# Kernel optimization log

Hardware: AMD Instinct MI355X
Metric: run time of the kernel (lower is better)

Reference implementation:

```python
import jax, jax.numpy as jnp
import numpy as np

OUT, IN, BLK = 4096, 4096, 32
N_BLOCKS = OUT * IN // BLK
# FP4 magnitude lookup (E2M1): index = low 3 bits of the nibble
FP4_LOOKUP = jnp.array([0.0, 0.5, 1.0, 1.5, 2.0, 3.0, 4.0, 6.0], dtype=jnp.float32)


def setup_inputs() -> dict:
    key = jax.random.key(0)
    k1, k2, k3, k4 = jax.random.split(key, 4)
    x = jax.random.normal(k1, (4, 2048, IN), dtype=jnp.float32)
    # packed uint8 codes (stored as int32): two FP4 nibbles per byte
    quantized_weight = jax.random.randint(k2, (OUT * IN // 2,), 0, 256, dtype=jnp.int32)
    # positive per-block scales (abs-max of each 32-element block in the original)
    weight_scales = jax.random.uniform(k3, (N_BLOCKS,), dtype=jnp.float32, minval=0.01, maxval=1.0)
    bias = jax.random.normal(k4, (OUT,), dtype=jnp.float32) * 0.01
    return {"x": x, "quantized_weight": quantized_weight,
            "weight_scales": weight_scales, "bias": bias}


def _dequantize(quantized_weight, weight_scales):
    # unpack: high nibble first, then low nibble (matches _unpack_fp4 stack order)
    high = (quantized_weight >> 4) & 15
    low = quantized_weight & 15
    nibbles = jnp.stack([high, low], axis=-1).reshape(-1)  # [OUT*IN]
    # sign bit (bit 3): 1 -> negative, 0 -> positive
    sign = jnp.where(((nibbles >> 3) & 1) == 1, -1.0, 1.0).astype(jnp.float32)
    magnitude = FP4_LOOKUP[nibbles & 7]
    vals = magnitude * sign                                  # [OUT*IN]
    vals = vals.reshape(N_BLOCKS, BLK) * weight_scales[:, None]
    return vals.reshape(OUT, IN)


def reference(x, quantized_weight, weight_scales, bias):
    W = _dequantize(quantized_weight, weight_scales)  # [OUT, IN]
    # F.linear: x @ W.T + bias
    return jnp.einsum('bsi,oi->bso', x, W) + bias
```

## Files before the change

### kernel.cpp

```cpp
#include <hip/hip_runtime.h>
#include <hip/hip_bf16.h>
#include <stdint.h>


#define M_DIM 8192
#define N_DIM 4096
#define K_DIM 4096
#define NBLK_W (N_DIM * K_DIM / 32)

typedef __bf16 bf16x8 __attribute__((ext_vector_type(8)));
typedef float  f32x4  __attribute__((ext_vector_type(4)));


__device__ __forceinline__ uint16_t f32_to_bf16_rn(float f) {
  uint32_t u = __float_as_uint(f);
  uint32_t r = (u + 0x7FFFu + ((u >> 16) & 1u)) >> 16;
  return (uint16_t)r;
}
__device__ __forceinline__ uint32_t pack_bf16x2(float e0, float e1) {
  return (uint32_t)f32_to_bf16_rn(e0) | ((uint32_t)f32_to_bf16_rn(e1) << 16);
}
__device__ __forceinline__ float fp4_to_f32(int nib) {
  uint32_t e = (uint32_t)(nib >> 1) & 3u;
  uint32_t m = (uint32_t)nib & 1u;
  uint32_t s = (uint32_t)(nib >> 3) & 1u;
  uint32_t bits = e ? (((126u + e) << 23) | (m << 22)) : (m ? 0x3F000000u : 0u);
  bits |= s << 31;
  return __uint_as_float(bits);
}
__device__ __forceinline__ void gload_lds16(const void* g, void* lds) {
  __builtin_amdgcn_global_load_lds(
      (const __attribute__((address_space(1))) unsigned int*)g,
      (__attribute__((address_space(3))) unsigned int*)lds,
      16, 0, 0);
}

__global__ __launch_bounds__(256) void dequant_w(const int* __restrict__ q,
                                                 const float* __restrict__ scales,
                                                 uint32_t* __restrict__ W) {
  int b = blockIdx.x * 256 + threadIdx.x;
  float sc = scales[b];
  const int4* q4 = reinterpret_cast<const int4*>(q) + (size_t)b * 4;
  int4* dst = reinterpret_cast<int4*>(W + (size_t)b * 16);
#pragma unroll
  for (int i = 0; i < 4; ++i) {
    int4 v = q4[i];
    int b0 = v.x & 0xFF, b1 = v.y & 0xFF, b2 = v.z & 0xFF, b3 = v.w & 0xFF;
    uint32_t p0 = pack_bf16x2(fp4_to_f32((b0 >> 4) & 15) * sc, fp4_to_f32(b0 & 15) * sc);
    uint32_t p1 = pack_bf16x2(fp4_to_f32((b1 >> 4) & 15) * sc, fp4_to_f32(b1 & 15) * sc);
    uint32_t p2 = pack_bf16x2(fp4_to_f32((b2 >> 4) & 15) * sc, fp4_to_f32(b2 & 15) * sc);
    uint32_t p3 = pack_bf16x2(fp4_to_f32((b3 >> 4) & 15) * sc, fp4_to_f32(b3 & 15) * sc);
    int4 o; o.x = (int)p0; o.y = (int)p1; o.z = (int)p2; o.w = (int)p3;
    dst[i] = o;
  }
}

__global__ __launch_bounds__(256) void cvt_x(const float* __restrict__ x,
                                             uint32_t* __restrict__ xb) {
  size_t i = ((size_t)blockIdx.x * 256 + threadIdx.x) * 8;
  float4 a = *reinterpret_cast<const float4*>(x + i);
  float4 c = *reinterpret_cast<const float4*>(x + i + 4);
  int4 o;
  o.x = (int)pack_bf16x2(a.x, a.y);
  o.y = (int)pack_bf16x2(a.z, a.w);
  o.z = (int)pack_bf16x2(c.x, c.y);
  o.w = (int)pack_bf16x2(c.z, c.w);
  *reinterpret_cast<int4*>(xb + i / 2) = o;
}


#define BUF0 0
#define BUF1 65536
#define A0OFF 0
#define A1OFF 16384
#define B0OFF 32768
#define B1OFF 49152
#define AH1 (128 * 4096)
#define NITER 32

#define BARRIER()   asm volatile("s_barrier" ::: "memory")
#define WAIT_LGKM0() do { asm volatile("s_waitcnt lgkmcnt(0)" ::: "memory"); \
                          __builtin_amdgcn_sched_barrier(0); } while (0)
#define WAIT_VM4()  asm volatile("s_waitcnt vmcnt(4)" ::: "memory")
#define WAIT_VM0()  asm volatile("s_waitcnt vmcnt(0)" ::: "memory")

template <int P>
__device__ __forceinline__ void phase_lda(bf16x8 (&aA)[2][2], const char* sm,
                                          int cb, uint32_t a_rd) {
  const uint32_t r0 = a_rd + (2 * P) * 2048;
  const uint32_t r1 = a_rd + (2 * P + 1) * 2048;
  aA[0][0] = *(const bf16x8*)(sm + cb + r0);
  aA[0][1] = *(const bf16x8*)(sm + cb + (r0 ^ 64));
  aA[1][0] = *(const bf16x8*)(sm + cb + r1);
  aA[1][1] = *(const bf16x8*)(sm + cb + (r1 ^ 64));
}

__device__ __forceinline__ void phase_ldb(bf16x8 (&bfr)[4][2], const char* sm,
                                          int cb, uint32_t b_rd) {
#pragma unroll
  for (int nf = 0; nf < 4; ++nf) {
    const uint32_t r = b_rd + nf * 2048;
    bfr[nf][0] = *(const bf16x8*)(sm + cb + r);
    bfr[nf][1] = *(const bf16x8*)(sm + cb + (r ^ 64));
  }
}

template <int P>
__device__ __forceinline__ void phase_mfma(f32x4 (&acc)[8][4],
                                           const bf16x8 (&aA)[2][2],
                                           const bf16x8 (&bfr)[4][2]) {
#pragma unroll
  for (int nf = 0; nf < 4; ++nf)
#pragma unroll
    for (int kk = 0; kk < 2; ++kk) {
      acc[2 * P][nf] = __builtin_amdgcn_mfma_f32_16x16x32_bf16(
          aA[0][kk], bfr[nf][kk], acc[2 * P][nf], 0, 0, 0);
      acc[2 * P + 1][nf] = __builtin_amdgcn_mfma_f32_16x16x32_bf16(
          aA[1][kk], bfr[nf][kk], acc[2 * P + 1][nf], 0, 0, 0);
    }
}

__device__ __forceinline__ void stage_half_tile(const __bf16* gsrc, char* lds_dst) {
  gload_lds16(gsrc, lds_dst);
  gload_lds16(gsrc + 64 * 4096, lds_dst + 8192);
}

#define PHASE(CB, P, STAGE, TAIL)            \
  do {                                       \
    phase_lda<P>(aA, smem, CB, a_rd);        \
    if ((P) == 0) phase_ldb(bfr, smem, CB, b_rd); \
    STAGE                                    \
    BARRIER();                               \
    WAIT_LGKM0();                            \
    __builtin_amdgcn_s_setprio(1);           \
    phase_mfma<P>(acc, aA, bfr);             \
    __builtin_amdgcn_s_setprio(0);           \
    TAIL                                     \
    BARRIER();                               \
  } while (0)

__global__ __launch_bounds__(512, 2) void gemm256_8ph(const __bf16* __restrict__ A,
                                                      const __bf16* __restrict__ B,
                                                      const float* __restrict__ bias,
                                                      float* __restrict__ C) {
  __shared__ __align__(16) char smem[131072];

  const int t    = threadIdx.x;
  const int wave = t >> 6;
  const int lane = t & 63;
  const int l16  = lane & 15;
  const int kg   = lane >> 4;
  const int wm   = wave >> 2;
  const int wn   = wave & 3;

  const int orig = blockIdx.x;
  const int swz  = (orig & 7) * 64 + (orig >> 3);
  const int bn   = swz & 15;
  const int bm   = swz >> 4;

  const int c8 = (t & 7) ^ ((t >> 3) & 7);
  const __bf16* gA = A + ((size_t)(bm * 256 + (t >> 3))) * 4096 + c8 * 8;
  const __bf16* gB = B + ((size_t)(bn * 256 + (t >> 3))) * 4096 + c8 * 8;
  char* stw = smem + wave * 1024;

  const uint32_t ca = ((uint32_t)(kg ^ (l16 & 7))) << 4;
  const uint32_t a_rd = (uint32_t)(wm ? A1OFF : A0OFF) + (uint32_t)l16 * 128 + ca;
  const uint32_t b_rd = (uint32_t)(wn >= 2 ? B1OFF : B0OFF) +
                        (uint32_t)(wn & 1) * 8192 + (uint32_t)l16 * 128 + ca;

  f32x4 acc[8][4];
#pragma unroll
  for (int i = 0; i < 8; ++i)
#pragma unroll
    for (int j = 0; j < 4; ++j) acc[i][j] = (f32x4){0.f, 0.f, 0.f, 0.f};

  bf16x8 aA[2][2];
  bf16x8 bfr[4][2];

  stage_half_tile(gA,             stw + BUF0 + A0OFF);
  stage_half_tile(gA + AH1,       stw + BUF0 + A1OFF);
  stage_half_tile(gB,             stw + BUF0 + B0OFF);
  stage_half_tile(gB + AH1,       stw + BUF0 + B1OFF);
  stage_half_tile(gB + 64,        stw + BUF1 + B0OFF);
  stage_half_tile(gB + AH1 + 64,  stw + BUF1 + B1OFF);
  WAIT_VM4();
  BARRIER();

  for (int j = 0; j < NITER - 1; ++j) {
    const size_t kO  = (size_t)(2 * j + 1) * 64;
    const size_t kE2 = (size_t)(2 * j + 2) * 64;
    const size_t kO2 = (size_t)(2 * j + 3) * 64;
    PHASE(BUF0, 0, stage_half_tile(gA + kO,        stw + BUF1 + A0OFF);, );
    PHASE(BUF0, 1, stage_half_tile(gA + AH1 + kO,  stw + BUF1 + A1OFF);, );
    PHASE(BUF0, 2, stage_half_tile(gB + kE2,       stw + BUF0 + B0OFF);, );
    PHASE(BUF0, 3, stage_half_tile(gB + AH1 + kE2, stw + BUF0 + B1OFF);, WAIT_VM4(););
    PHASE(BUF1, 0, stage_half_tile(gA + kE2,       stw + BUF0 + A0OFF);, );
    PHASE(BUF1, 1, stage_half_tile(gA + AH1 + kE2, stw + BUF0 + A1OFF);, );
    PHASE(BUF1, 2, stage_half_tile(gB + kO2,       stw + BUF1 + B0OFF);, );
    PHASE(BUF1, 3, stage_half_tile(gB + AH1 + kO2, stw + BUF1 + B1OFF);, WAIT_VM4(););
  }
  {
    const size_t kO = (size_t)(2 * (NITER - 1) + 1) * 64;
    PHASE(BUF0, 0, stage_half_tile(gA + kO,       stw + BUF1 + A0OFF);, );
    PHASE(BUF0, 1, stage_half_tile(gA + AH1 + kO, stw + BUF1 + A1OFF);, );
    PHASE(BUF0, 2, ;, );
    PHASE(BUF0, 3, ;, WAIT_VM0(););
    PHASE(BUF1, 0, ;, );
    PHASE(BUF1, 1, ;, );
    PHASE(BUF1, 2, ;, );
    PHASE(BUF1, 3, ;, );
  }

#pragma unroll
  for (int mf = 0; mf < 8; ++mf) {
    const int m0 = bm * 256 + wm * 128 + mf * 16 + kg * 4;
#pragma unroll
    for (int nf = 0; nf < 4; ++nf) {
      const int n = bn * 256 + wn * 64 + nf * 16 + l16;
      const float bv = bias[n];
#pragma unroll
      for (int r = 0; r < 4; ++r)
        C[(size_t)(m0 + r) * N_DIM + n] = acc[mf][nf][r] + bv;
    }
  }
}

__global__ __launch_bounds__(256) void naive_fused(const float* __restrict__ x,
                                                   const int* __restrict__ q,
                                                   const float* __restrict__ scales,
                                                   const float* __restrict__ bias,
                                                   float* __restrict__ out) {
  __shared__ float xs[K_DIM];
  const int m = blockIdx.y;
  const int n = blockIdx.x * 256 + threadIdx.x;
  for (int k = threadIdx.x; k < K_DIM; k += 256)
    xs[k] = x[(size_t)m * K_DIM + k];
  __syncthreads();

  const int4* q4 = reinterpret_cast<const int4*>(q) + (size_t)n * 512;
  float acc = 0.f, sc = 0.f;
  for (int c = 0; c < 512; ++c) {
    if ((c & 3) == 0) sc = scales[n * 128 + (c >> 2)];
    int4 v = q4[c];
    int b0 = v.x & 0xFF, b1 = v.y & 0xFF, b2 = v.z & 0xFF, b3 = v.w & 0xFF;
    int k = c * 8;
    acc += xs[k + 0] * fp4_to_f32((b0 >> 4) & 15) * sc;
    acc += xs[k + 1] * fp4_to_f32(b0 & 15) * sc;
    acc += xs[k + 2] * fp4_to_f32((b1 >> 4) & 15) * sc;
    acc += xs[k + 3] * fp4_to_f32(b1 & 15) * sc;
    acc += xs[k + 4] * fp4_to_f32((b2 >> 4) & 15) * sc;
    acc += xs[k + 5] * fp4_to_f32(b2 & 15) * sc;
    acc += xs[k + 6] * fp4_to_f32((b3 >> 4) & 15) * sc;
    acc += xs[k + 7] * fp4_to_f32(b3 & 15) * sc;
  }
  out[(size_t)m * N_DIM + n] = acc + bias[n];
}

extern "C" void kernel_launch(void* const* d_in, const int* in_sizes, int n_in,
                              void* d_out, int out_size, void* d_ws, size_t ws_size,
                              hipStream_t stream) {
  const float* x    = (const float*)d_in[0];
  const int*   q    = (const int*)d_in[1];
  const float* sc   = (const float*)d_in[2];
  const float* bias = (const float*)d_in[3];
  float* out = (float*)d_out;

  const size_t xb_bytes = (size_t)M_DIM * K_DIM * 2;
  const size_t w_bytes  = (size_t)N_DIM * K_DIM * 2;

  if (ws_size >= xb_bytes + w_bytes) {
    uint32_t* xb = (uint32_t*)d_ws;
    uint32_t* W  = (uint32_t*)((char*)d_ws + xb_bytes);

    dequant_w<<<NBLK_W / 256, 256, 0, stream>>>(q, sc, W);
    cvt_x<<<(M_DIM * (size_t)K_DIM / 8) / 256, 256, 0, stream>>>(x, xb);

    gemm256_8ph<<<dim3(512), 512, 0, stream>>>((const __bf16*)xb, (const __bf16*)W, bias, out);
  } else {
    dim3 grid(N_DIM / 256, M_DIM);
    naive_fused<<<grid, 256, 0, stream>>>(x, q, sc, bias, out);
  }
}
```

Baseline: 284.9 us.

## Double-buffer A fragments in registers to overlap LDS reads with MFMA

Restructures the 8-phase GEMM main loop so A-operand LDS reads for the next phase are issued before the current phase's MFMAs, using two register sets for A fragments. It removes one barrier per phase and reorders global-to-LDS staging, including prefetching the next A tile earlier, with adjusted vmcnt waits. The goal is to hide LDS latency behind matrix math, at the cost of more VGPRs and a riskier synchronisation schedule.

```diff
diff --git a/kernel.cpp b/kernel.cpp
--- a/kernel.cpp
+++ b/kernel.cpp
@@ -81,63 +81,49 @@
 #define BARRIER()   asm volatile("s_barrier" ::: "memory")
 #define WAIT_LGKM0() do { asm volatile("s_waitcnt lgkmcnt(0)" ::: "memory"); \
                           __builtin_amdgcn_sched_barrier(0); } while (0)
+#define LGKM4()     do { asm volatile("s_waitcnt lgkmcnt(4)" ::: "memory"); \
+                          __builtin_amdgcn_sched_barrier(0); } while (0)
+#define WAIT_VM6()  asm volatile("s_waitcnt vmcnt(6)" ::: "memory")
 #define WAIT_VM4()  asm volatile("s_waitcnt vmcnt(4)" ::: "memory")
 #define WAIT_VM0()  asm volatile("s_waitcnt vmcnt(0)" ::: "memory")
-
-template <int P>
-__device__ __forceinline__ void phase_lda(bf16x8 (&aA)[2][2], const char* sm,
-                                          int cb, uint32_t a_rd) {
-  const uint32_t r0 = a_rd + (2 * P) * 2048;
-  const uint32_t r1 = a_rd + (2 * P + 1) * 2048;
-  aA[0][0] = *(const bf16x8*)(sm + cb + r0);
-  aA[0][1] = *(const bf16x8*)(sm + cb + (r0 ^ 64));
-  aA[1][0] = *(const bf16x8*)(sm + cb + r1);
-  aA[1][1] = *(const bf16x8*)(sm + cb + (r1 ^ 64));
-}
-
-__device__ __forceinline__ void phase_ldb(bf16x8 (&bfr)[4][2], const char* sm,
-                                          int cb, uint32_t b_rd) {
-#pragma unroll
-  for (int nf = 0; nf < 4; ++nf) {
-    const uint32_t r = b_rd + nf * 2048;
-    bfr[nf][0] = *(const bf16x8*)(sm + cb + r);
-    bfr[nf][1] = *(const bf16x8*)(sm + cb + (r ^ 64));
-  }
-}
-
-template <int P>
-__device__ __forceinline__ void phase_mfma(f32x4 (&acc)[8][4],
-                                           const bf16x8 (&aA)[2][2],
-                                           const bf16x8 (&bfr)[4][2]) {
-#pragma unroll
-  for (int nf = 0; nf < 4; ++nf)
-#pragma unroll
-    for (int kk = 0; kk < 2; ++kk) {
-      acc[2 * P][nf] = __builtin_amdgcn_mfma_f32_16x16x32_bf16(
-          aA[0][kk], bfr[nf][kk], acc[2 * P][nf], 0, 0, 0);
-      acc[2 * P + 1][nf] = __builtin_amdgcn_mfma_f32_16x16x32_bf16(
-          aA[1][kk], bfr[nf][kk], acc[2 * P + 1][nf], 0, 0, 0);
-    }
-}
+#define PRIO1()     __builtin_amdgcn_s_setprio(1)
+#define PRIO0()     __builtin_amdgcn_s_setprio(0)
+
+#define LDA2(SET, CB, F) do {                                      \
+    const uint32_t r0_ = a_rd + (F) * 2048;                        \
+    const uint32_t r1_ = a_rd + ((F) + 1) * 2048;                  \
+    aA[SET][0][0] = *(const bf16x8*)(smem + (CB) + r0_);           \
+    aA[SET][0][1] = *(const bf16x8*)(smem + (CB) + (r0_ ^ 64));    \
+    aA[SET][1][0] = *(const bf16x8*)(smem + (CB) + r1_);           \
+    aA[SET][1][1] = *(const bf16x8*)(smem + (CB) + (r1_ ^ 64));    \
+  } while (0)
+
+#define LDB(CB) do {                                               \
+    _Pragma("unroll")                                              \
+    for (int nf_ = 0; nf_ < 4; ++nf_) {                            \
+      const uint32_t r_ = b_rd + nf_ * 2048;                       \
+      bfr[nf_][0] = *(const bf16x8*)(smem + (CB) + r_);            \
+      bfr[nf_][1] = *(const bf16x8*)(smem + (CB) + (r_ ^ 64));     \
+    }                                                              \
+  } while (0)
+
+#define MFMAQ(Q, SET) do {                                         \
+    _Pragma("unroll")                                              \
+    for (int nf_ = 0; nf_ < 4; ++nf_) {                            \
+      _Pragma("unroll")                                            \
+      for (int kk_ = 0; kk_ < 2; ++kk_) {                          \
+        acc[2*(Q)][nf_] = __builtin_amdgcn_mfma_f32_16x16x32_bf16( \
+            aA[SET][0][kk_], bfr[nf_][kk_], acc[2*(Q)][nf_], 0, 0, 0);   \
+        acc[2*(Q)+1][nf_] = __builtin_amdgcn_mfma_f32_16x16x32_bf16(     \
+            aA[SET][1][kk_], bfr[nf_][kk_], acc[2*(Q)+1][nf_], 0, 0, 0); \
+      }                                                            \
+    }                                                              \
+  } while (0)
 
 __device__ __forceinline__ void stage_half_tile(const __bf16* gsrc, char* lds_dst) {
   gload_lds16(gsrc, lds_dst);
   gload_lds16(gsrc + 64 * 4096, lds_dst + 8192);
 }
-
-#define PHASE(CB, P, STAGE, TAIL)            \
-  do {                                       \
-    phase_lda<P>(aA, smem, CB, a_rd);        \
-    if ((P) == 0) phase_ldb(bfr, smem, CB, b_rd); \
-    STAGE                                    \
-    BARRIER();                               \
-    WAIT_LGKM0();                            \
-    __builtin_amdgcn_s_setprio(1);           \
-    phase_mfma<P>(acc, aA, bfr);             \
-    __builtin_amdgcn_s_setprio(0);           \
-    TAIL                                     \
-    BARRIER();                               \
-  } while (0)
 
 __global__ __launch_bounds__(512, 2) void gemm256_8ph(const __bf16* __restrict__ A,
                                                       const __bf16* __restrict__ B,
@@ -174,41 +160,98 @@
 #pragma unroll
     for (int j = 0; j < 4; ++j) acc[i][j] = (f32x4){0.f, 0.f, 0.f, 0.f};
 
-  bf16x8 aA[2][2];
+  bf16x8 aA[2][2][2];
   bf16x8 bfr[4][2];
 
-  stage_half_tile(gA,             stw + BUF0 + A0OFF);
-  stage_half_tile(gA + AH1,       stw + BUF0 + A1OFF);
-  stage_half_tile(gB,             stw + BUF0 + B0OFF);
-  stage_half_tile(gB + AH1,       stw + BUF0 + B1OFF);
-  stage_half_tile(gB + 64,        stw + BUF1 + B0OFF);
-  stage_half_tile(gB + AH1 + 64,  stw + BUF1 + B1OFF);
-  WAIT_VM4();
+  stage_half_tile(gA,            stw + BUF0 + A0OFF);
+  stage_half_tile(gA + AH1,      stw + BUF0 + A1OFF);
+  stage_half_tile(gB,            stw + BUF0 + B0OFF);
+  stage_half_tile(gB + AH1,      stw + BUF0 + B1OFF);
+  stage_half_tile(gB + 64,       stw + BUF1 + B0OFF);
+  stage_half_tile(gB + AH1 + 64, stw + BUF1 + B1OFF);
+  stage_half_tile(gA + 64,       stw + BUF1 + A0OFF);
+  WAIT_VM6();
   BARRIER();
+  LDA2(0, BUF0, 0);
 
   for (int j = 0; j < NITER - 1; ++j) {
     const size_t kO  = (size_t)(2 * j + 1) * 64;
     const size_t kE2 = (size_t)(2 * j + 2) * 64;
     const size_t kO2 = (size_t)(2 * j + 3) * 64;
-    PHASE(BUF0, 0, stage_half_tile(gA + kO,        stw + BUF1 + A0OFF);, );
-    PHASE(BUF0, 1, stage_half_tile(gA + AH1 + kO,  stw + BUF1 + A1OFF);, );
-    PHASE(BUF0, 2, stage_half_tile(gB + kE2,       stw + BUF0 + B0OFF);, );
-    PHASE(BUF0, 3, stage_half_tile(gB + AH1 + kE2, stw + BUF0 + B1OFF);, WAIT_VM4(););
-    PHASE(BUF1, 0, stage_half_tile(gA + kE2,       stw + BUF0 + A0OFF);, );
-    PHASE(BUF1, 1, stage_half_tile(gA + AH1 + kE2, stw + BUF0 + A1OFF);, );
-    PHASE(BUF1, 2, stage_half_tile(gB + kO2,       stw + BUF1 + B0OFF);, );
-    PHASE(BUF1, 3, stage_half_tile(gB + AH1 + kO2, stw + BUF1 + B1OFF);, WAIT_VM4(););
+    WAIT_LGKM0();
+    LDB(BUF0);
+    LDA2(1, BUF0, 2);
+    LGKM4();
+    PRIO1(); MFMAQ(0, 0); PRIO0();
+    stage_half_tile(gA + AH1 + kO, stw + BUF1 + A1OFF);
+    BARRIER();
+    WAIT_LGKM0();
+    LDA2(0, BUF0, 4);
+    PRIO1(); MFMAQ(1, 1); PRIO0();
+    stage_half_tile(gB + kE2, stw + BUF0 + B0OFF);
+    BARRIER();
+    WAIT_LGKM0();
+    LDA2(1, BUF0, 6);
+    PRIO1(); MFMAQ(2, 0); PRIO0();
+    stage_half_tile(gB + AH1 + kE2, stw + BUF0 + B1OFF);
+    WAIT_VM4();
+    BARRIER();
+    WAIT_LGKM0();
+    LDA2(0, BUF1, 0);
+    PRIO1(); MFMAQ(3, 1); PRIO0();
+    stage_half_tile(gA + kE2, stw + BUF0 + A0OFF);
+    BARRIER();
+    WAIT_LGKM0();
+    LDB(BUF1);
+    LDA2(1, BUF1, 2);
+    LGKM4();
+    PRIO1(); MFMAQ(0, 0); PRIO0();
+    stage_half_tile(gA + AH1 + kE2, stw + BUF0 + A1OFF);
+    BARRIER();
+    WAIT_LGKM0();
+    LDA2(0, BUF1, 4);
+    PRIO1(); MFMAQ(1, 1); PRIO0();
+    stage_half_tile(gB + kO2, stw + BUF1 + B0OFF);
+    BARRIER();
+    WAIT_LGKM0();
+    LDA2(1, BUF1, 6);
+    PRIO1(); MFMAQ(2, 0); PRIO0();
+    stage_half_tile(gB + AH1 + kO2, stw + BUF1 + B1OFF);
+    stage_half_tile(gA + kO2,       stw + BUF1 + A0OFF);
+    WAIT_VM6();
+    BARRIER();
+    WAIT_LGKM0();
+    LDA2(0, BUF0, 0);
+    PRIO1(); MFMAQ(3, 1); PRIO0();
+    BARRIER();
   }
   {
     const size_t kO = (size_t)(2 * (NITER - 1) + 1) * 64;
-    PHASE(BUF0, 0, stage_half_tile(gA + kO,       stw + BUF1 + A0OFF);, );
-    PHASE(BUF0, 1, stage_half_tile(gA + AH1 + kO, stw + BUF1 + A1OFF);, );
-    PHASE(BUF0, 2, ;, );
-    PHASE(BUF0, 3, ;, WAIT_VM0(););
-    PHASE(BUF1, 0, ;, );
-    PHASE(BUF1, 1, ;, );
-    PHASE(BUF1, 2, ;, );
-    PHASE(BUF1, 3, ;, );
+    WAIT_LGKM0(); LDB(BUF0); LDA2(1, BUF0, 2); LGKM4();
+    PRIO1(); MFMAQ(0, 0); PRIO0();
+    stage_half_tile(gA + AH1 + kO, stw + BUF1 + A1OFF);
+    BARRIER();
+    WAIT_LGKM0(); LDA2(0, BUF0, 4);
+    PRIO1(); MFMAQ(1, 1); PRIO0();
+    BARRIER();
+    WAIT_LGKM0(); LDA2(1, BUF0, 6);
+    PRIO1(); MFMAQ(2, 0); PRIO0();
+    WAIT_VM0();
+    BARRIER();
+    WAIT_LGKM0(); LDA2(0, BUF1, 0);
+    PRIO1(); MFMAQ(3, 1); PRIO0();
+    BARRIER();
+    WAIT_LGKM0(); LDB(BUF1); LDA2(1, BUF1, 2); LGKM4();
+    PRIO1(); MFMAQ(0, 0); PRIO0();
+    BARRIER();
+    WAIT_LGKM0(); LDA2(0, BUF1, 4);
+    PRIO1(); MFMAQ(1, 1); PRIO0();
+    BARRIER();
+    WAIT_LGKM0(); LDA2(1, BUF1, 6);
+    PRIO1(); MFMAQ(2, 0); PRIO0();
+    BARRIER();
+    WAIT_LGKM0();
+    PRIO1(); MFMAQ(3, 1); PRIO0();
   }
 
 #pragma unroll
```

Measured after the change: 282.0 us. Within noise of the previous version (-1.0%).
